# Performance work log

Hardware: AMD Instinct MI355X
Metric: run time of the kernel (lower is better)

Reference implementation:

```python
import jax, jax.numpy as jnp
import numpy as np

N_OBJ, N_P, N2 = 16, 128, 2048
C, H, W = 256, 384, 384
IMG_W, IMG_H = 384.0, 384.0  # img_metas['img_shape'][:2][::-1]
SIM_THR = 0.0
LOSS_WEIGHT = 1.0
COS_EPS = 1e-8  # torch F.cosine_similarity default


def setup_inputs() -> dict:
    key = jax.random.key(0)
    k1, k2, k3, k4 = jax.random.split(key, 4)
    img_size = jnp.array([IMG_W, IMG_H], jnp.float32)
    point_set_1 = jax.random.uniform(k1, (N_OBJ, N_P, 2), jnp.float32) * img_size
    point_set_2 = jax.random.uniform(k2, (N_OBJ, N2, 2), jnp.float32) * img_size
    key_points = jax.random.uniform(k3, (N_OBJ * N_P, 2), jnp.float32) * img_size
    feats = jax.random.normal(k4, (1, C, H, W), jnp.float32)
    return {"point_set_1": point_set_1, "point_set_2": point_set_2,
            "feats": feats, "key_points": key_points}


def _grid_sample(img, pts01):
    # img: [C,H,W]; pts01: [P,2] (x,y) in [0,1]. Bilinear, align_corners=False,
    # zero padding -- matches mmcv point_sample / torch grid_sample.
    Ci, Hi, Wi = img.shape
    g = 2.0 * pts01 - 1.0
    x = ((g[:, 0] + 1.0) * Wi - 1.0) * 0.5
    y = ((g[:, 1] + 1.0) * Hi - 1.0) * 0.5
    x0 = jnp.floor(x)
    y0 = jnp.floor(y)
    wx1 = x - x0
    wy1 = y - y0

    def tap(xi, yi, wgt):
        valid = (xi >= 0) & (xi < Wi) & (yi >= 0) & (yi < Hi)
        xc = jnp.clip(xi, 0, Wi - 1).astype(jnp.int32)
        yc = jnp.clip(yi, 0, Hi - 1).astype(jnp.int32)
        return img[:, yc, xc] * (wgt * valid)[None, :]  # [C,P]

    return (tap(x0, y0, (1 - wx1) * (1 - wy1))
            + tap(x0 + 1, y0, wx1 * (1 - wy1))
            + tap(x0, y0 + 1, (1 - wx1) * wy1)
            + tap(x0 + 1, y0 + 1, wx1 * wy1))  # [C,P]


def reference(point_set_1, point_set_2, feats, key_points):
    img_size = jnp.array([IMG_W, IMG_H], feats.dtype)
    img = feats[0]  # feats.expand() reuses the same map for every object

    # feats_set_1: [n_obj, n_p, C]; feats_set_2: [n_obj, n2, C]
    f1 = _grid_sample(img, key_points / img_size).T.reshape(N_OBJ, N_P, C)
    f2 = _grid_sample(img, (point_set_2 / img_size).reshape(-1, 2)).T.reshape(N_OBJ, N2, C)

    # cosine similarity over channel dim (norms clamped to eps like torch)
    n1 = jnp.maximum(jnp.linalg.norm(f1, axis=-1), COS_EPS)  # [O,P]
    n2 = jnp.maximum(jnp.linalg.norm(f2, axis=-1), COS_EPS)  # [O,N2]
    sims = jnp.einsum('opc,onc->opn', f1, f2) / (n1[..., None] * n2[:, None, :])
    mask = sims >= SIM_THR  # [O,P,N2]

    # pairwise L2 distances between each key point and candidate set
    diff = point_set_1[:, :, None, :] - point_set_2[:, None, :, :]
    d = jnp.linalg.norm(diff, axis=-1)  # [O,P,N2]

    cnt = mask.sum(-1)  # [O,P]
    has = cnt > 0
    dmin = jnp.min(jnp.where(mask, d, jnp.inf), axis=-1)
    dmean = jnp.sum(jnp.where(mask, d, 0.0), axis=-1) / jnp.maximum(cnt, 1)
    # chamfer of a single point vs masked set: (nearest + mean)/2, 'mean' reduction
    m = (point_set_2.sum(axis=(1, 2)) >= 0).astype(d.dtype)  # [O]
    cost = jnp.where(has, 0.5 * (dmin + dmean), 0.0) * m[:, None]  # [O,P]

    dist = (cost.sum(-1) / N_P).mean()
    return dist * LOSS_WEIGHT
```

## Files before the change

kernel.cpp:

```cpp
#include <hip/hip_runtime.h>
#include <hip/hip_bf16.h>
#include <math.h>

#define W_    384
#define H_    384
#define HW_   (384*384)
#define C_    256
#define NOBJ  16
#define NP    128
#define N2    2048
#define IMGW  384.0f
#define IMGH  384.0f
#define NCH   32

__global__ __launch_bounds__(256) void k_transpose(const float* __restrict__ feats,
                                                   unsigned short* __restrict__ ftT) {
    __shared__ float tile[64][65];
    int b     = blockIdx.x;
    int pbase = (b % (HW_ / 64)) * 64;
    int cbase = (b / (HW_ / 64)) * 64;
    int lane  = threadIdx.x & 63;
    int grp   = threadIdx.x >> 6;

    #pragma unroll
    for (int r = 0; r < 16; ++r) {
        int c = r * 4 + grp;
        tile[c][lane] = feats[(size_t)(cbase + c) * HW_ + pbase + lane];
    }
    __syncthreads();
    #pragma unroll
    for (int r = 0; r < 16; ++r) {
        int p = r * 4 + grp;
        float v = tile[lane][p];
        unsigned int u = __float_as_uint(v);
        u += 0x7fffu + ((u >> 16) & 1u);
        ftT[(size_t)(pbase + p) * C_ + cbase + lane] = (unsigned short)(u >> 16);
    }
}

__global__ __launch_bounds__(256) void k_sample(const float* __restrict__ pts, int npts,
                                                const unsigned short* __restrict__ ftT,
                                                float* __restrict__ out) {
    int point = blockIdx.x * 4 + (threadIdx.x >> 6);
    if (point >= npts) return;
    int lane  = threadIdx.x & 63;
    int cb    = lane * 4;

    float px = pts[point * 2 + 0];
    float py = pts[point * 2 + 1];
    float x  = px * ((float)W_ / IMGW) - 0.5f;
    float y  = py * ((float)H_ / IMGH) - 0.5f;
    float x0 = floorf(x), y0 = floorf(y);
    int ix0 = (int)x0, iy0 = (int)y0;
    float fx = x - x0, fy = y - y0;

    float a0 = 0.f, a1 = 0.f, a2 = 0.f, a3 = 0.f;
    #pragma unroll
    for (int dy = 0; dy < 2; ++dy) {
        #pragma unroll
        for (int dx = 0; dx < 2; ++dx) {
            int ix = ix0 + dx, iy = iy0 + dy;
            float w = (dx ? fx : 1.f - fx) * (dy ? fy : 1.f - fy);
            if (ix >= 0 && ix < W_ && iy >= 0 && iy < H_) {
                const ushort4 t = *(const ushort4*)(ftT + ((size_t)(iy * W_ + ix) * C_ + cb));
                a0 += w * __uint_as_float((unsigned)t.x << 16);
                a1 += w * __uint_as_float((unsigned)t.y << 16);
                a2 += w * __uint_as_float((unsigned)t.z << 16);
                a3 += w * __uint_as_float((unsigned)t.w << 16);
            }
        }
    }
    float4 o; o.x = a0; o.y = a1; o.z = a2; o.w = a3;
    *(float4*)(out + (size_t)point * C_ + cb) = o;
}

__global__ __launch_bounds__(256) void k_sample_direct(const float* __restrict__ pts, int npts,
                                                       const float* __restrict__ feats,
                                                       float* __restrict__ out) {
    int point = blockIdx.x * 4 + (threadIdx.x >> 6);
    if (point >= npts) return;
    int lane  = threadIdx.x & 63;
    int cb    = lane * 4;

    float px = pts[point * 2 + 0];
    float py = pts[point * 2 + 1];
    float x  = px * ((float)W_ / IMGW) - 0.5f;
    float y  = py * ((float)H_ / IMGH) - 0.5f;
    float x0 = floorf(x), y0 = floorf(y);
    int ix0 = (int)x0, iy0 = (int)y0;
    float fx = x - x0, fy = y - y0;

    float acc[4] = {0.f, 0.f, 0.f, 0.f};
    #pragma unroll
    for (int dy = 0; dy < 2; ++dy) {
        #pragma unroll
        for (int dx = 0; dx < 2; ++dx) {
            int ix = ix0 + dx, iy = iy0 + dy;
            float w = (dx ? fx : 1.f - fx) * (dy ? fy : 1.f - fy);
            if (ix >= 0 && ix < W_ && iy >= 0 && iy < H_) {
                int base = iy * W_ + ix;
                #pragma unroll
                for (int u = 0; u < 4; ++u)
                    acc[u] += w * feats[(size_t)(cb + u) * HW_ + base];
            }
        }
    }
    float4 o; o.x = acc[0]; o.y = acc[1]; o.z = acc[2]; o.w = acc[3];
    *(float4*)(out + (size_t)point * C_ + cb) = o;
}

__global__ __launch_bounds__(256) void k_simdist(const float* __restrict__ f1,
                                                 const float* __restrict__ f2,
                                                 const float* __restrict__ ps1,
                                                 const float* __restrict__ ps2,
                                                 float* __restrict__ pmin,
                                                 float* __restrict__ psum,
                                                 float* __restrict__ pcnt) {
    __shared__ __align__(16) float As[16][64];
    __shared__ __align__(16) float Bs[16][64];
    __shared__ float s1x[64], s1y[64], s2x[64], s2y[64];

    int b  = blockIdx.x;
    int o  = b >> 6;
    int pc = (b >> 5) & 1;
    int nc = b & 31;
    int pbase = pc * 64, nbase = nc * 64;
    int t  = threadIdx.x;

    if (t < 64) {
        const float* q = ps1 + (size_t)(o * NP + pbase + t) * 2;
        s1x[t] = q[0]; s1y[t] = q[1];
    } else if (t < 128) {
        int n = t - 64;
        const float* q = ps2 + (size_t)(o * N2 + nbase + n) * 2;
        s2x[n] = q[0]; s2y[n] = q[1];
    }

    int tx = t & 15, ty = t >> 4;
    float acc[4][4] = {};

    int lrow = t >> 2;
    int lk   = (t & 3) * 4;
    const float* aptr = f1 + ((size_t)(o * NP + pbase + lrow) * C_ + lk);
    const float* bptr = f2 + ((size_t)(o * N2 + nbase + lrow) * C_ + lk);

    for (int kb = 0; kb < C_; kb += 16) {
        float4 av = *(const float4*)(aptr + kb);
        float4 bv = *(const float4*)(bptr + kb);
        __syncthreads();
        As[lk + 0][lrow] = av.x; As[lk + 1][lrow] = av.y;
        As[lk + 2][lrow] = av.z; As[lk + 3][lrow] = av.w;
        Bs[lk + 0][lrow] = bv.x; Bs[lk + 1][lrow] = bv.y;
        Bs[lk + 2][lrow] = bv.z; Bs[lk + 3][lrow] = bv.w;
        __syncthreads();
        #pragma unroll
        for (int kk = 0; kk < 16; ++kk) {
            float4 a4 = *(const float4*)&As[kk][ty * 4];
            float4 b4 = *(const float4*)&Bs[kk][tx * 4];
            acc[0][0] += a4.x * b4.x; acc[0][1] += a4.x * b4.y;
            acc[0][2] += a4.x * b4.z; acc[0][3] += a4.x * b4.w;
            acc[1][0] += a4.y * b4.x; acc[1][1] += a4.y * b4.y;
            acc[1][2] += a4.y * b4.z; acc[1][3] += a4.y * b4.w;
            acc[2][0] += a4.z * b4.x; acc[2][1] += a4.z * b4.y;
            acc[2][2] += a4.z * b4.z; acc[2][3] += a4.z * b4.w;
            acc[3][0] += a4.w * b4.x; acc[3][1] += a4.w * b4.y;
            acc[3][2] += a4.w * b4.z; acc[3][3] += a4.w * b4.w;
        }
    }

    #pragma unroll
    for (int i = 0; i < 4; ++i) {
        int pl = ty * 4 + i;
        float px = s1x[pl], py = s1y[pl];
        float mn = INFINITY, sm = 0.f, ct = 0.f;
        #pragma unroll
        for (int j = 0; j < 4; ++j) {
            int nl = tx * 4 + j;
            if (acc[i][j] >= 0.f) {
                float dx = px - s2x[nl], dy = py - s2y[nl];
                float d  = sqrtf(dx * dx + dy * dy);
                mn = fminf(mn, d); sm += d; ct += 1.f;
            }
        }
        #pragma unroll
        for (int off = 1; off < 16; off <<= 1) {
            mn = fminf(mn, __shfl_xor(mn, off, 16));
            sm += __shfl_xor(sm, off, 16);
            ct += __shfl_xor(ct, off, 16);
        }
        if (tx == 0) {
            int idx = (o * NCH + nc) * NP + pbase + pl;
            pmin[idx] = mn; psum[idx] = sm; pcnt[idx] = ct;
        }
    }
}

__global__ __launch_bounds__(256) void k_final(const float* __restrict__ pmin,
                                               const float* __restrict__ psum,
                                               const float* __restrict__ pcnt,
                                               float* __restrict__ out) {
    int t = threadIdx.x;
    float tot = 0.f;
    for (int pair = t; pair < NOBJ * NP; pair += 256) {
        int o = pair >> 7, p = pair & 127;
        float mn = INFINITY, sm = 0.f, ct = 0.f;
        for (int ch = 0; ch < NCH; ++ch) {
            int idx = (o * NCH + ch) * NP + p;
            mn = fminf(mn, pmin[idx]);
            sm += psum[idx];
            ct += pcnt[idx];
        }
        if (ct > 0.f) tot += 0.5f * (mn + sm / ct);
    }
    #pragma unroll
    for (int off = 32; off; off >>= 1) tot += __shfl_xor(tot, off, 64);
    __shared__ float wsum[4];
    if ((t & 63) == 0) wsum[t >> 6] = tot;
    __syncthreads();
    if (t == 0)
        out[0] = (wsum[0] + wsum[1] + wsum[2] + wsum[3]) * (1.0f / (NOBJ * NP));
}

extern "C" void kernel_launch(void* const* d_in, const int* in_sizes, int n_in,
                              void* d_out, int out_size, void* d_ws, size_t ws_size,
                              hipStream_t stream) {
    const float* ps1   = (const float*)d_in[0];
    const float* ps2   = (const float*)d_in[1];
    const float* feats = (const float*)d_in[2];
    const float* kpts  = (const float*)d_in[3];
    float* out = (float*)d_out;

    const size_t sz_ftT  = (size_t)HW_ * C_ * sizeof(unsigned short);
    const size_t sz_f1   = (size_t)NOBJ * NP * C_ * sizeof(float);
    const size_t sz_f2   = (size_t)NOBJ * N2 * C_ * sizeof(float);
    const size_t sz_part = (size_t)NOBJ * NCH * NP * sizeof(float);
    const size_t need_full = sz_ftT + sz_f1 + sz_f2 + 3 * sz_part;

    char* ws = (char*)d_ws;
    if (ws_size >= need_full) {
        unsigned short* ftT = (unsigned short*)ws;
        float* f1   = (float*)(ws + sz_ftT);
        float* f2   = (float*)(ws + sz_ftT + sz_f1);
        float* pmin = (float*)(ws + sz_ftT + sz_f1 + sz_f2);
        float* psum = (float*)(ws + sz_ftT + sz_f1 + sz_f2 + sz_part);
        float* pcnt = (float*)(ws + sz_ftT + sz_f1 + sz_f2 + 2 * sz_part);

        k_transpose<<<(HW_ / 64) * (C_ / 64), 256, 0, stream>>>(feats, ftT);
        k_sample<<<(NOBJ * NP) / 4, 256, 0, stream>>>(kpts, NOBJ * NP, ftT, f1);
        k_sample<<<(NOBJ * N2) / 4, 256, 0, stream>>>(ps2, NOBJ * N2, ftT, f2);
        k_simdist<<<NOBJ * 2 * NCH, 256, 0, stream>>>(f1, f2, ps1, ps2, pmin, psum, pcnt);
        k_final<<<1, 256, 0, stream>>>(pmin, psum, pcnt, out);
    } else {
        float* f1   = (float*)ws;
        float* f2   = (float*)(ws + sz_f1);
        float* pmin = (float*)(ws + sz_f1 + sz_f2);
        float* psum = (float*)(ws + sz_f1 + sz_f2 + sz_part);
        float* pcnt = (float*)(ws + sz_f1 + sz_f2 + 2 * sz_part);

        k_sample_direct<<<(NOBJ * NP) / 4, 256, 0, stream>>>(kpts, NOBJ * NP, feats, f1);
        k_sample_direct<<<(NOBJ * N2) / 4, 256, 0, stream>>>(ps2, NOBJ * N2, feats, f2);
        k_simdist<<<NOBJ * 2 * NCH, 256, 0, stream>>>(f1, f2, ps1, ps2, pmin, psum, pcnt);
        k_final<<<1, 256, 0, stream>>>(pmin, psum, pcnt, out);
    }
}
```

Before: 303.9 us.

## Use bf16 MFMA for similarity GEMM and merge sample launches

Rewrites the similarity kernel to compute the sign of dot products with bf16 MFMA 16x16x32 instructions per wavefront. Sampled features are stored as bf16 in one combined buffer, which halves their memory traffic. The two sampling launches are merged into one. Only the sign of the similarity is needed, so bf16 rounding may flip mask decisions for dot products near zero.

```diff
diff --git a/kernel.cpp b/kernel.cpp
--- a/kernel.cpp
+++ b/kernel.cpp
@@ -9,9 +9,13 @@
 #define NOBJ  16
 #define NP    128
 #define N2    2048
-#define IMGW  384.0f
-#define IMGH  384.0f
-#define NCH   32
+#define NF1   (NOBJ*NP)
+#define NPTS  (NOBJ*NP + NOBJ*N2)
+#define NG    16
+#define NT    8
+
+typedef __attribute__((ext_vector_type(8))) short short8;
+typedef __attribute__((ext_vector_type(4))) float f32x4;
 
 __global__ __launch_bounds__(256) void k_transpose(const float* __restrict__ feats,
                                                    unsigned short* __restrict__ ftT) {
@@ -31,25 +35,25 @@
     #pragma unroll
     for (int r = 0; r < 16; ++r) {
         int p = r * 4 + grp;
-        float v = tile[lane][p];
-        unsigned int u = __float_as_uint(v);
+        unsigned int u = __float_as_uint(tile[lane][p]);
         u += 0x7fffu + ((u >> 16) & 1u);
         ftT[(size_t)(pbase + p) * C_ + cbase + lane] = (unsigned short)(u >> 16);
     }
 }
 
-__global__ __launch_bounds__(256) void k_sample(const float* __restrict__ pts, int npts,
+__global__ __launch_bounds__(256) void k_sample(const float* __restrict__ kpts,
+                                                const float* __restrict__ ps2,
                                                 const unsigned short* __restrict__ ftT,
-                                                float* __restrict__ out) {
+                                                unsigned short* __restrict__ f12) {
     int point = blockIdx.x * 4 + (threadIdx.x >> 6);
-    if (point >= npts) return;
     int lane  = threadIdx.x & 63;
     int cb    = lane * 4;
 
-    float px = pts[point * 2 + 0];
-    float py = pts[point * 2 + 1];
-    float x  = px * ((float)W_ / IMGW) - 0.5f;
-    float y  = py * ((float)H_ / IMGH) - 0.5f;
+    const float* src = (point < NF1) ? (kpts + (size_t)point * 2)
+                                     : (ps2 + (size_t)(point - NF1) * 2);
+    float px = src[0], py = src[1];
+    float x  = px - 0.5f;
+    float y  = py - 0.5f;
     float x0 = floorf(x), y0 = floorf(y);
     int ix0 = (int)x0, iy0 = (int)y0;
     float fx = x - x0, fy = y - y0;
@@ -70,22 +74,27 @@
             }
         }
     }
-    float4 o; o.x = a0; o.y = a1; o.z = a2; o.w = a3;
-    *(float4*)(out + (size_t)point * C_ + cb) = o;
-}
-
-__global__ __launch_bounds__(256) void k_sample_direct(const float* __restrict__ pts, int npts,
+    ushort4 o;
+    unsigned u;
+    u = __float_as_uint(a0); u += 0x7fffu + ((u >> 16) & 1u); o.x = (unsigned short)(u >> 16);
+    u = __float_as_uint(a1); u += 0x7fffu + ((u >> 16) & 1u); o.y = (unsigned short)(u >> 16);
+    u = __float_as_uint(a2); u += 0x7fffu + ((u >> 16) & 1u); o.z = (unsigned short)(u >> 16);
+    u = __float_as_uint(a3); u += 0x7fffu + ((u >> 16) & 1u); o.w = (unsigned short)(u >> 16);
+    *(ushort4*)(f12 + (size_t)point * C_ + cb) = o;
+}
+
+__global__ __launch_bounds__(256) void k_sample_direct(const float* __restrict__ kpts,
+                                                       const float* __restrict__ ps2,
                                                        const float* __restrict__ feats,
-                                                       float* __restrict__ out) {
+                                                       unsigned short* __restrict__ f12) {
     int point = blockIdx.x * 4 + (threadIdx.x >> 6);
-    if (point >= npts) return;
     int lane  = threadIdx.x & 63;
     int cb    = lane * 4;
 
-    float px = pts[point * 2 + 0];
-    float py = pts[point * 2 + 1];
-    float x  = px * ((float)W_ / IMGW) - 0.5f;
-    float y  = py * ((float)H_ / IMGH) - 0.5f;
+    const float* src = (point < NF1) ? (kpts + (size_t)point * 2)
+                                     : (ps2 + (size_t)(point - NF1) * 2);
+    float px = src[0], py = src[1];
+    float x  = px - 0.5f, y = py - 0.5f;
     float x0 = floorf(x), y0 = floorf(y);
     int ix0 = (int)x0, iy0 = (int)y0;
     float fx = x - x0, fy = y - y0;
@@ -105,92 +114,83 @@
             }
         }
     }
-    float4 o; o.x = acc[0]; o.y = acc[1]; o.z = acc[2]; o.w = acc[3];
-    *(float4*)(out + (size_t)point * C_ + cb) = o;
-}
-
-__global__ __launch_bounds__(256) void k_simdist(const float* __restrict__ f1,
-                                                 const float* __restrict__ f2,
+    ushort4 o;
+    unsigned u;
+    u = __float_as_uint(acc[0]); u += 0x7fffu + ((u >> 16) & 1u); o.x = (unsigned short)(u >> 16);
+    u = __float_as_uint(acc[1]); u += 0x7fffu + ((u >> 16) & 1u); o.y = (unsigned short)(u >> 16);
+    u = __float_as_uint(acc[2]); u += 0x7fffu + ((u >> 16) & 1u); o.z = (unsigned short)(u >> 16);
+    u = __float_as_uint(acc[3]); u += 0x7fffu + ((u >> 16) & 1u); o.w = (unsigned short)(u >> 16);
+    *(ushort4*)(f12 + (size_t)point * C_ + cb) = o;
+}
+
+__global__ __launch_bounds__(256) void k_simdist(const unsigned short* __restrict__ f12,
                                                  const float* __restrict__ ps1,
                                                  const float* __restrict__ ps2,
                                                  float* __restrict__ pmin,
                                                  float* __restrict__ psum,
                                                  float* __restrict__ pcnt) {
-    __shared__ __align__(16) float As[16][64];
-    __shared__ __align__(16) float Bs[16][64];
-    __shared__ float s1x[64], s1y[64], s2x[64], s2y[64];
-
-    int b  = blockIdx.x;
-    int o  = b >> 6;
-    int pc = (b >> 5) & 1;
-    int nc = b & 31;
-    int pbase = pc * 64, nbase = nc * 64;
-    int t  = threadIdx.x;
-
-    if (t < 64) {
-        const float* q = ps1 + (size_t)(o * NP + pbase + t) * 2;
-        s1x[t] = q[0]; s1y[t] = q[1];
-    } else if (t < 128) {
-        int n = t - 64;
-        const float* q = ps2 + (size_t)(o * N2 + nbase + n) * 2;
-        s2x[n] = q[0]; s2y[n] = q[1];
-    }
-
-    int tx = t & 15, ty = t >> 4;
-    float acc[4][4] = {};
-
-    int lrow = t >> 2;
-    int lk   = (t & 3) * 4;
-    const float* aptr = f1 + ((size_t)(o * NP + pbase + lrow) * C_ + lk);
-    const float* bptr = f2 + ((size_t)(o * N2 + nbase + lrow) * C_ + lk);
-
-    for (int kb = 0; kb < C_; kb += 16) {
-        float4 av = *(const float4*)(aptr + kb);
-        float4 bv = *(const float4*)(bptr + kb);
-        __syncthreads();
-        As[lk + 0][lrow] = av.x; As[lk + 1][lrow] = av.y;
-        As[lk + 2][lrow] = av.z; As[lk + 3][lrow] = av.w;
-        Bs[lk + 0][lrow] = bv.x; Bs[lk + 1][lrow] = bv.y;
-        Bs[lk + 2][lrow] = bv.z; Bs[lk + 3][lrow] = bv.w;
-        __syncthreads();
-        #pragma unroll
-        for (int kk = 0; kk < 16; ++kk) {
-            float4 a4 = *(const float4*)&As[kk][ty * 4];
-            float4 b4 = *(const float4*)&Bs[kk][tx * 4];
-            acc[0][0] += a4.x * b4.x; acc[0][1] += a4.x * b4.y;
-            acc[0][2] += a4.x * b4.z; acc[0][3] += a4.x * b4.w;
-            acc[1][0] += a4.y * b4.x; acc[1][1] += a4.y * b4.y;
-            acc[1][2] += a4.y * b4.z; acc[1][3] += a4.y * b4.w;
-            acc[2][0] += a4.z * b4.x; acc[2][1] += a4.z * b4.y;
-            acc[2][2] += a4.z * b4.z; acc[2][3] += a4.z * b4.w;
-            acc[3][0] += a4.w * b4.x; acc[3][1] += a4.w * b4.y;
-            acc[3][2] += a4.w * b4.z; acc[3][3] += a4.w * b4.w;
-        }
-    }
-
-    #pragma unroll
-    for (int i = 0; i < 4; ++i) {
-        int pl = ty * 4 + i;
-        float px = s1x[pl], py = s1y[pl];
-        float mn = INFINITY, sm = 0.f, ct = 0.f;
-        #pragma unroll
-        for (int j = 0; j < 4; ++j) {
-            int nl = tx * 4 + j;
-            if (acc[i][j] >= 0.f) {
-                float dx = px - s2x[nl], dy = py - s2y[nl];
+    int wid  = blockIdx.x * 4 + (threadIdx.x >> 6);
+    int lane = threadIdx.x & 63;
+    int ng = wid & 15;
+    int pt = (wid >> 4) & 7;
+    int o  = wid >> 7;
+    int quad = lane >> 4, col = lane & 15;
+
+    const short* f12s = (const short*)f12;
+    const short8* aptr =
+        (const short8*)(f12s + ((size_t)(o * NP + pt * 16 + col) * C_ + quad * 8));
+    short8 a[8];
+    #pragma unroll
+    for (int kb = 0; kb < 8; ++kb) a[kb] = aptr[kb * 4];
+
+    const float2* ps1v = (const float2*)ps1;
+    const float2* ps2v = (const float2*)ps2;
+    float pxr[4], pyr[4];
+    #pragma unroll
+    for (int r = 0; r < 4; ++r) {
+        float2 pc = ps1v[o * NP + pt * 16 + quad * 4 + r];
+        pxr[r] = pc.x; pyr[r] = pc.y;
+    }
+
+    float mn[4] = {INFINITY, INFINITY, INFINITY, INFINITY};
+    float sm[4] = {0.f, 0.f, 0.f, 0.f};
+    float ct[4] = {0.f, 0.f, 0.f, 0.f};
+
+    for (int t = 0; t < NT; ++t) {
+        int nbase = ng * 128 + t * 16;
+        const short8* bptr =
+            (const short8*)(f12s + ((size_t)(NF1 + o * N2 + nbase + col) * C_ + quad * 8));
+        f32x4 acc = {0.f, 0.f, 0.f, 0.f};
+        #pragma unroll
+        for (int kb = 0; kb < 8; ++kb)
+            acc = __builtin_amdgcn_mfma_f32_16x16x32_bf16(a[kb], bptr[kb * 4], acc, 0, 0, 0);
+
+        float2 nc = ps2v[o * N2 + nbase + col];
+        #pragma unroll
+        for (int r = 0; r < 4; ++r) {
+            if (acc[r] >= 0.f) {
+                float dx = pxr[r] - nc.x, dy = pyr[r] - nc.y;
                 float d  = sqrtf(dx * dx + dy * dy);
-                mn = fminf(mn, d); sm += d; ct += 1.f;
+                mn[r] = fminf(mn[r], d); sm[r] += d; ct[r] += 1.f;
             }
         }
+    }
+
+    #pragma unroll
+    for (int r = 0; r < 4; ++r) {
         #pragma unroll
         for (int off = 1; off < 16; off <<= 1) {
-            mn = fminf(mn, __shfl_xor(mn, off, 16));
-            sm += __shfl_xor(sm, off, 16);
-            ct += __shfl_xor(ct, off, 16);
-        }
-        if (tx == 0) {
-            int idx = (o * NCH + nc) * NP + pbase + pl;
-            pmin[idx] = mn; psum[idx] = sm; pcnt[idx] = ct;
+            mn[r] = fminf(mn[r], __shfl_xor(mn[r], off, 16));
+            sm[r] += __shfl_xor(sm[r], off, 16);
+            ct[r] += __shfl_xor(ct[r], off, 16);
+        }
+    }
+    if (col == 0) {
+        #pragma unroll
+        for (int r = 0; r < 4; ++r) {
+            int p   = pt * 16 + quad * 4 + r;
+            int idx = (o * NG + ng) * NP + p;
+            pmin[idx] = mn[r]; psum[idx] = sm[r]; pcnt[idx] = ct[r];
         }
     }
 }
@@ -204,8 +204,8 @@
     for (int pair = t; pair < NOBJ * NP; pair += 256) {
         int o = pair >> 7, p = pair & 127;
         float mn = INFINITY, sm = 0.f, ct = 0.f;
-        for (int ch = 0; ch < NCH; ++ch) {
-            int idx = (o * NCH + ch) * NP + p;
+        for (int g = 0; g < NG; ++g) {
+            int idx = (o * NG + g) * NP + p;
             mn = fminf(mn, pmin[idx]);
             sm += psum[idx];
             ct += pcnt[idx];
@@ -231,35 +231,29 @@
     float* out = (float*)d_out;
 
     const size_t sz_ftT  = (size_t)HW_ * C_ * sizeof(unsigned short);
-    const size_t sz_f1   = (size_t)NOBJ * NP * C_ * sizeof(float);
-    const size_t sz_f2   = (size_t)NOBJ * N2 * C_ * sizeof(float);
-    const size_t sz_part = (size_t)NOBJ * NCH * NP * sizeof(float);
-    const size_t need_full = sz_ftT + sz_f1 + sz_f2 + 3 * sz_part;
+    const size_t sz_f12  = (size_t)NPTS * C_ * sizeof(unsigned short);
+    const size_t sz_part = (size_t)NOBJ * NG * NP * sizeof(float);
 
     char* ws = (char*)d_ws;
-    if (ws_size >= need_full) {
+    if (ws_size >= sz_ftT + sz_f12 + 3 * sz_part) {
         unsigned short* ftT = (unsigned short*)ws;
-        float* f1   = (float*)(ws + sz_ftT);
-        float* f2   = (float*)(ws + sz_ftT + sz_f1);
-        float* pmin = (float*)(ws + sz_ftT + sz_f1 + sz_f2);
-        float* psum = (float*)(ws + sz_ftT + sz_f1 + sz_f2 + sz_part);
-        float* pcnt = (float*)(ws + sz_ftT + sz_f1 + sz_f2 + 2 * sz_part);
+        unsigned short* f12 = (unsigned short*)(ws + sz_ftT);
+        float* pmin = (float*)(ws + sz_ftT + sz_f12);
+        float* psum = (float*)(ws + sz_ftT + sz_f12 + sz_part);
+        float* pcnt = (float*)(ws + sz_ftT + sz_f12 + 2 * sz_part);
 
         k_transpose<<<(HW_ / 64) * (C_ / 64), 256, 0, stream>>>(feats, ftT);
-        k_sample<<<(NOBJ * NP) / 4, 256, 0, stream>>>(kpts, NOBJ * NP, ftT, f1);
-        k_sample<<<(NOBJ * N2) / 4, 256, 0, stream>>>(ps2, NOBJ * N2, ftT, f2);
-        k_simdist<<<NOBJ * 2 * NCH, 256, 0, stream>>>(f1, f2, ps1, ps2, pmin, psum, pcnt);
+        k_sample<<<NPTS / 4, 256, 0, stream>>>(kpts, ps2, ftT, f12);
+        k_simdist<<<NOBJ * 8 * NG / 4, 256, 0, stream>>>(f12, ps1, ps2, pmin, psum, pcnt);
         k_final<<<1, 256, 0, stream>>>(pmin, psum, pcnt, out);
     } else {
-        float* f1   = (float*)ws;
-        float* f2   = (float*)(ws + sz_f1);
-        float* pmin = (float*)(ws + sz_f1 + sz_f2);
-        float* psum = (float*)(ws + sz_f1 + sz_f2 + sz_part);
-        float* pcnt = (float*)(ws + sz_f1 + sz_f2 + 2 * sz_part);
-
-        k_sample_direct<<<(NOBJ * NP) / 4, 256, 0, stream>>>(kpts, NOBJ * NP, feats, f1);
-        k_sample_direct<<<(NOBJ * N2) / 4, 256, 0, stream>>>(ps2, NOBJ * N2, feats, f2);
-        k_simdist<<<NOBJ * 2 * NCH, 256, 0, stream>>>(f1, f2, ps1, ps2, pmin, psum, pcnt);
+        unsigned short* f12 = (unsigned short*)ws;
+        float* pmin = (float*)(ws + sz_f12);
+        float* psum = (float*)(ws + sz_f12 + sz_part);
+        float* pcnt = (float*)(ws + sz_f12 + 2 * sz_part);
+
+        k_sample_direct<<<NPTS / 4, 256, 0, stream>>>(kpts, ps2, feats, f12);
+        k_simdist<<<NOBJ * 8 * NG / 4, 256, 0, stream>>>(f12, ps1, ps2, pmin, psum, pcnt);
         k_final<<<1, 256, 0, stream>>>(pmin, psum, pcnt, out);
     }
 }
```

New measurement: 277.7 us. -8.6%, faster.
